# Optimization experiments

Hardware: AMD Instinct MI355X
Metric: run time of the kernel (lower is better)

The kernel has to match this reference:

```python
import jax, jax.numpy as jnp
import numpy as np

B, L = 512, 8192

def setup_inputs() -> dict:
    key = jax.random.key(0)
    k1, k2, k3 = jax.random.split(key, 3)
    # one-hot labels [B, L, 2] (original code tests y_true[...] == 1.0)
    labels = jax.random.randint(k1, (B, L), 0, 2)
    y_true = jax.nn.one_hot(labels, 2, dtype=jnp.float32)
    # predicted probabilities in (0, 1) so log is finite
    y_pred = jax.random.uniform(k2, (B, L, 2), dtype=jnp.float32, minval=1e-4, maxval=1.0)
    doc_len = jax.random.randint(k3, (B,), 1, L + 1).astype(jnp.int32)
    return {"y_true": y_true, "y_pred": y_pred, "doc_len": doc_len}

def reference(y_true, y_pred, doc_len):
    diminish_factor = 1.0  # forward default
    # valid-position mask [B, L] replaces the per-sample python loop + slicing
    valid = jnp.arange(y_pred.shape[1])[None, :] < doc_len[:, None]
    logp = jnp.log(y_pred)  # [B, L, 2]
    pos_sel = valid & (y_true[..., 1] == 1.0)
    neg_sel = valid & (y_true[..., 0] == 1.0)
    pos_loss = -jnp.sum(jnp.where(pos_sel, logp[..., 1], 0.0))
    neg_loss = -jnp.sum(jnp.where(neg_sel, logp[..., 0], 0.0)) * diminish_factor
    total_len = jnp.sum(doc_len).astype(logp.dtype)
    return (pos_loss + neg_loss) / total_len
```

## Files before the change

kernel.cpp:

```cpp
#include <hip/hip_runtime.h>


#define BLOCK 256
#define POS_PER_THREAD 8
#define POS_PER_BLOCK (BLOCK * POS_PER_THREAD)

__global__ __launch_bounds__(BLOCK) void ce_main(
    const float* __restrict__ y_true,
    const float* __restrict__ y_pred,
    const int*   __restrict__ doc_len,
    float*       __restrict__ partials,
    int L, int chunks_per_row)
{
    const int b     = blockIdx.x / chunks_per_row;
    const int chunk = blockIdx.x % chunks_per_row;
    const int dl    = doc_len[b];

    const int start = chunk * POS_PER_BLOCK;
    if (start >= dl) {
        if (threadIdx.x == 0) partials[blockIdx.x] = 0.0f;
        return;
    }

    const size_t row_base = (size_t)b * L;
    float local = 0.0f;

    #pragma unroll
    for (int j = 0; j < POS_PER_THREAD / 2; ++j) {
        const int pos = start + j * (BLOCK * 2) + (int)threadIdx.x * 2;
        if (pos < dl) {
            const size_t e = (row_base + (size_t)pos) * 2;
            const float4 t = *(const float4*)(y_true + e);
            const float4 p = *(const float4*)(y_pred + e);
            local += t.x * (-__logf(p.x)) + t.y * (-__logf(p.y));
            if (pos + 1 < dl) {
                local += t.z * (-__logf(p.z)) + t.w * (-__logf(p.w));
            }
        }
    }

    #pragma unroll
    for (int off = 32; off > 0; off >>= 1)
        local += __shfl_down(local, off, 64);

    __shared__ float wsum[BLOCK / 64];
    const int lane = threadIdx.x & 63;
    const int wid  = threadIdx.x >> 6;
    if (lane == 0) wsum[wid] = local;
    __syncthreads();
    if (threadIdx.x == 0) {
        float s = 0.0f;
        #pragma unroll
        for (int w = 0; w < BLOCK / 64; ++w) s += wsum[w];
        partials[blockIdx.x] = s;
    }
}

__global__ __launch_bounds__(BLOCK) void ce_finalize(
    const float* __restrict__ partials, int npart,
    const int*   __restrict__ doc_len,  int B,
    float*       __restrict__ out)
{
    float s = 0.0f;
    if ((npart & 3) == 0) {
        const float4* p4 = (const float4*)partials;
        const int n4 = npart >> 2;
        for (int i = threadIdx.x; i < n4; i += BLOCK) {
            const float4 v = p4[i];
            s += (v.x + v.y) + (v.z + v.w);
        }
    } else {
        for (int i = threadIdx.x; i < npart; i += BLOCK)
            s += partials[i];
    }

    int len = 0;
    for (int i = threadIdx.x; i < B; i += BLOCK)
        len += doc_len[i];

    #pragma unroll
    for (int off = 32; off > 0; off >>= 1) {
        s   += __shfl_down(s, off, 64);
        len += __shfl_down(len, off, 64);
    }

    __shared__ float fsum[BLOCK / 64];
    __shared__ int   isum[BLOCK / 64];
    const int lane = threadIdx.x & 63;
    const int wid  = threadIdx.x >> 6;
    if (lane == 0) { fsum[wid] = s; isum[wid] = len; }
    __syncthreads();
    if (threadIdx.x == 0) {
        float fs = 0.0f; int is = 0;
        #pragma unroll
        for (int w = 0; w < BLOCK / 64; ++w) { fs += fsum[w]; is += isum[w]; }
        out[0] = fs / (float)is;
    }
}

extern "C" void kernel_launch(void* const* d_in, const int* in_sizes, int n_in,
                              void* d_out, int out_size, void* d_ws, size_t ws_size,
                              hipStream_t stream)
{
    const float* y_true  = (const float*)d_in[0];
    const float* y_pred  = (const float*)d_in[1];
    const int*   doc_len = (const int*)d_in[2];
    float*       out     = (float*)d_out;
    float*       ws      = (float*)d_ws;

    const int B = in_sizes[2];
    const int L = in_sizes[0] / (2 * B);
    const int chunks_per_row = (L + POS_PER_BLOCK - 1) / POS_PER_BLOCK;
    const int npart = B * chunks_per_row;

    ce_main<<<dim3(npart), BLOCK, 0, stream>>>(y_true, y_pred, doc_len, ws, L, chunks_per_row);
    ce_finalize<<<dim3(1), BLOCK, 0, stream>>>(ws, npart, doc_len, B, out);
}
```

Measured before the change: 94.93 us.

## Fuse main and finalize into one cooperative persistent kernel with grid sync

Replaces the two-kernel reduction with a single cooperative kernel on a fixed grid of 1024 blocks that loops over chunks, then uses a grid-wide sync so block 0 does the final reduction. It also adds a fast path for full chunks with nontemporal loads and two accumulators. The aim is to remove the second launch and reduce the number of blocks, at the cost of grid-sync overhead and the constraints of a cooperative launch.

```diff
diff --git a/kernel.cpp b/kernel.cpp
--- a/kernel.cpp
+++ b/kernel.cpp
@@ -1,44 +1,62 @@
 #include <hip/hip_runtime.h>
+#include <hip/hip_cooperative_groups.h>
+
+namespace cg = cooperative_groups;
 
 
 #define BLOCK 256
+#define GRID  1024
 #define POS_PER_THREAD 8
 #define POS_PER_BLOCK (BLOCK * POS_PER_THREAD)
 
-__global__ __launch_bounds__(BLOCK) void ce_main(
+typedef float f32x4 __attribute__((ext_vector_type(4)));
+
+__global__ __launch_bounds__(BLOCK, 4) void ce_fused(
     const float* __restrict__ y_true,
     const float* __restrict__ y_pred,
     const int*   __restrict__ doc_len,
     float*       __restrict__ partials,
-    int L, int chunks_per_row)
+    float*       __restrict__ out,
+    int L, int chunks_per_row, int total_chunks, int B)
 {
-    const int b     = blockIdx.x / chunks_per_row;
-    const int chunk = blockIdx.x % chunks_per_row;
-    const int dl    = doc_len[b];
+    float acc0 = 0.0f, acc1 = 0.0f;
 
-    const int start = chunk * POS_PER_BLOCK;
-    if (start >= dl) {
-        if (threadIdx.x == 0) partials[blockIdx.x] = 0.0f;
-        return;
-    }
+    for (int c = blockIdx.x; c < total_chunks; c += GRID) {
+        const int b     = c / chunks_per_row;
+        const int chunk = c - b * chunks_per_row;
+        const int dl    = doc_len[b];
+        const int start = chunk * POS_PER_BLOCK;
+        if (start >= dl) continue;
 
-    const size_t row_base = (size_t)b * L;
-    float local = 0.0f;
+        const size_t row2 = (size_t)b * (size_t)L * 2;
 
-    #pragma unroll
-    for (int j = 0; j < POS_PER_THREAD / 2; ++j) {
-        const int pos = start + j * (BLOCK * 2) + (int)threadIdx.x * 2;
-        if (pos < dl) {
-            const size_t e = (row_base + (size_t)pos) * 2;
-            const float4 t = *(const float4*)(y_true + e);
-            const float4 p = *(const float4*)(y_pred + e);
-            local += t.x * (-__logf(p.x)) + t.y * (-__logf(p.y));
-            if (pos + 1 < dl) {
-                local += t.z * (-__logf(p.z)) + t.w * (-__logf(p.w));
+        if (start + POS_PER_BLOCK <= dl) {
+            #pragma unroll
+            for (int j = 0; j < POS_PER_THREAD / 2; ++j) {
+                const int pos = start + j * (BLOCK * 2) + (int)threadIdx.x * 2;
+                const size_t e = row2 + (size_t)pos * 2;
+                const f32x4 t = __builtin_nontemporal_load((const f32x4*)(y_true + e));
+                const f32x4 p = __builtin_nontemporal_load((const f32x4*)(y_pred + e));
+                acc0 += t.x * (-__logf(p.x)) + t.y * (-__logf(p.y));
+                acc1 += t.z * (-__logf(p.z)) + t.w * (-__logf(p.w));
+            }
+        } else {
+            #pragma unroll
+            for (int j = 0; j < POS_PER_THREAD / 2; ++j) {
+                const int pos = start + j * (BLOCK * 2) + (int)threadIdx.x * 2;
+                if (pos < dl) {
+                    const size_t e = row2 + (size_t)pos * 2;
+                    const f32x4 t = *(const f32x4*)(y_true + e);
+                    const f32x4 p = *(const f32x4*)(y_pred + e);
+                    acc0 += t.x * (-__logf(p.x)) + t.y * (-__logf(p.y));
+                    if (pos + 1 < dl)
+                        acc1 += t.z * (-__logf(p.z)) + t.w * (-__logf(p.w));
+                }
             }
         }
     }
 
+    float local = acc0 + acc1;
     #pragma unroll
     for (int off = 32; off > 0; off >>= 1)
         local += __shfl_down(local, off, 64);
@@ -54,47 +72,36 @@
         for (int w = 0; w < BLOCK / 64; ++w) s += wsum[w];
         partials[blockIdx.x] = s;
     }
-}
 
-__global__ __launch_bounds__(BLOCK) void ce_finalize(
-    const float* __restrict__ partials, int npart,
-    const int*   __restrict__ doc_len,  int B,
-    float*       __restrict__ out)
-{
-    float s = 0.0f;
-    if ((npart & 3) == 0) {
-        const float4* p4 = (const float4*)partials;
-        const int n4 = npart >> 2;
-        for (int i = threadIdx.x; i < n4; i += BLOCK) {
-            const float4 v = p4[i];
-            s += (v.x + v.y) + (v.z + v.w);
+    __threadfence();
+    cg::this_grid().sync();
+
+    if (blockIdx.x == 0) {
+        float s = 0.0f;
+        #pragma unroll 4
+        for (int i = threadIdx.x; i < GRID; i += BLOCK)
+            s += partials[i];
+
+        int len = 0;
+        for (int i = threadIdx.x; i < B; i += BLOCK)
+            len += doc_len[i];
+
+        #pragma unroll
+        for (int off = 32; off > 0; off >>= 1) {
+            s   += __shfl_down(s, off, 64);
+            len += __shfl_down(len, off, 64);
         }
-    } else {
-        for (int i = threadIdx.x; i < npart; i += BLOCK)
-            s += partials[i];
-    }
 
-    int len = 0;
-    for (int i = threadIdx.x; i < B; i += BLOCK)
-        len += doc_len[i];
-
-    #pragma unroll
-    for (int off = 32; off > 0; off >>= 1) {
-        s   += __shfl_down(s, off, 64);
-        len += __shfl_down(len, off, 64);
-    }
-
-    __shared__ float fsum[BLOCK / 64];
-    __shared__ int   isum[BLOCK / 64];
-    const int lane = threadIdx.x & 63;
-    const int wid  = threadIdx.x >> 6;
-    if (lane == 0) { fsum[wid] = s; isum[wid] = len; }
-    __syncthreads();
-    if (threadIdx.x == 0) {
-        float fs = 0.0f; int is = 0;
-        #pragma unroll
-        for (int w = 0; w < BLOCK / 64; ++w) { fs += fsum[w]; is += isum[w]; }
-        out[0] = fs / (float)is;
+        __shared__ float fsum[BLOCK / 64];
+        __shared__ int   isum[BLOCK / 64];
+        if (lane == 0) { fsum[wid] = s; isum[wid] = len; }
+        __syncthreads();
+        if (threadIdx.x == 0) {
+            float fs = 0.0f; int is = 0;
+            #pragma unroll
+            for (int w = 0; w < BLOCK / 64; ++w) { fs += fsum[w]; is += isum[w]; }
+            out[0] = fs / (float)is;
+        }
     }
 }
 
@@ -108,11 +115,13 @@
     float*       out     = (float*)d_out;
     float*       ws      = (float*)d_ws;
 
-    const int B = in_sizes[2];
-    const int L = in_sizes[0] / (2 * B);
-    const int chunks_per_row = (L + POS_PER_BLOCK - 1) / POS_PER_BLOCK;
-    const int npart = B * chunks_per_row;
+    int B = in_sizes[2];
+    int L = in_sizes[0] / (2 * B);
+    int chunks_per_row = (L + POS_PER_BLOCK - 1) / POS_PER_BLOCK;
+    int total_chunks   = B * chunks_per_row;
 
-    ce_main<<<dim3(npart), BLOCK, 0, stream>>>(y_true, y_pred, doc_len, ws, L, chunks_per_row);
-    ce_finalize<<<dim3(1), BLOCK, 0, stream>>>(ws, npart, doc_len, B, out);
+    void* args[] = { &y_true, &y_pred, &doc_len, &ws, &out,
+                     &L, &chunks_per_row, &total_chunks, &B };
+    hipLaunchCooperativeKernel((const void*)ce_fused, dim3(GRID), dim3(BLOCK),
+                               args, 0, stream);
 }
```

Result: slower. 304.5 us (+220.7%).
